# Optimization experiments

Measured on AMD Instinct MI355X. Metric: run time of the kernel, lower is better.

## Reference

```python
import jax, jax.numpy as jnp
import numpy as np

V = 50257   # vocab_size
H = 1024    # hidden_size + 8
L = 2048    # input_length
ML = 2048   # max_length


def setup_inputs() -> dict:
    key = jax.random.key(0)
    ks = jax.random.split(key, 12)
    def w(k, shape, scale=0.02):
        return jax.random.normal(k, shape, dtype=jnp.float32) * scale
    return {
        'decoder_input': jax.random.randint(ks[0], (1, 1), 0, V),
        'hidden_state': jax.random.normal(ks[1], (1, 1, H), dtype=jnp.float32),
        'encoder_outputs': jax.random.normal(ks[2], (ML, H), dtype=jnp.float32),
        'input_variable': jax.random.randint(ks[3], (L, 1), 0, V),
        'embedding': w(ks[4], (V, H), 1.0),
        'W_attn_w': w(ks[5], (ML, 2 * H)), 'b_attn_w': jnp.zeros((ML,), jnp.float32),
        'W_attn_u': w(ks[6], (H, 2 * H)), 'b_attn_u': jnp.zeros((H,), jnp.float32),
        'W_ih': w(ks[7], (3 * H, H)), 'b_ih': jnp.zeros((3 * H,), jnp.float32),
        'W_hh': w(ks[8], (3 * H, H)), 'b_hh': jnp.zeros((3 * H,), jnp.float32),
        'W_copy': w(ks[9], (H, H)), 'b_copy': jnp.zeros((H,), jnp.float32),
        'W_gen': w(ks[10], (V, H)), 'b_gen': jnp.zeros((V,), jnp.float32),
    }


def _forward(decoder_input, hidden_state, encoder_outputs, input_variable,
             embedding, W_attn_w, b_attn_w, W_attn_u, b_attn_u,
             W_ih, b_ih, W_hh, b_hh, W_copy, b_copy, W_gen, b_gen):
    # batch_size = 1, single decode step (dropout is identity at inference)
    emb0 = embedding[decoder_input].reshape(1, H)           # (1, H)
    h0 = hidden_state[0]                                    # (1, H) previous hidden

    # attention over encoder outputs
    cat_eh = jnp.concatenate([emb0, h0], axis=1)            # (1, 2H)
    attn_weights = jax.nn.softmax(cat_eh @ W_attn_w.T + b_attn_w, axis=1)  # (1, ML)
    attn_applied = attn_weights @ encoder_outputs           # (1, H)

    joined = jnp.concatenate([emb0, attn_applied], axis=1)  # (1, 2H)
    rnn_in = jax.nn.relu(joined @ W_attn_u.T + b_attn_u)    # (1, H)

    # one GRU step (PyTorch gate layout: r, z, n)
    gi = rnn_in @ W_ih.T + b_ih                             # (1, 3H)
    gh = h0 @ W_hh.T + b_hh                                 # (1, 3H)
    r = jax.nn.sigmoid(gi[:, :H] + gh[:, :H])
    z = jax.nn.sigmoid(gi[:, H:2 * H] + gh[:, H:2 * H])
    n = jnp.tanh(gi[:, 2 * H:] + r * gh[:, 2 * H:])
    h_new = (1.0 - z) * n + z * h0                          # (1, H)
    final_hidden = h_new[None]                              # (1, 1, H)

    # generate + copy scores
    score_g = h_new @ W_gen.T + b_gen                       # (1, V)
    trimmed = encoder_outputs[:L]                           # (L, H)
    score_c = jnp.tanh(trimmed @ W_copy.T + b_copy) @ h0[0] # (L,)  bmm with OLD hidden
    probs = jax.nn.softmax(jnp.concatenate([score_g, score_c[None]], axis=1), axis=1)
    prob_g = probs[:, :V]                                   # (1, V)
    prob_c = probs[:, V:]                                   # (1, L)

    # copy->vocab: scatter-add (math-equivalent to dense one-hot bmm)
    idx = input_variable[:, 0]                              # (L,) int
    prob_c_to_g = jnp.zeros((V,), probs.dtype).at[idx].add(prob_c[0])[None]
    final_output = prob_g + prob_c_to_g                     # (1, V)

    # selective read: attend only to positions matching the current input token
    din = decoder_input[0, 0]
    matched = (idx == din).astype(probs.dtype)              # (L,)
    final_weights = ((prob_c * matched) @ trimmed)[:, None, :]  # (1, 1, H)
    return final_output, final_hidden, final_weights


def reference(decoder_input, hidden_state, encoder_outputs, input_variable,
              embedding, W_attn_w, b_attn_w, W_attn_u, b_attn_u,
              W_ih, b_ih, W_hh, b_hh, W_copy, b_copy, W_gen, b_gen):
    return _forward(decoder_input, hidden_state, encoder_outputs, input_variable,
                    embedding, W_attn_w, b_attn_w, W_attn_u, b_attn_u,
                    W_ih, b_ih, W_hh, b_hh, W_copy, b_copy, W_gen, b_gen)
```

## Files before the change

### kernel.cpp

```cpp
#include <hip/hip_runtime.h>
#include <math.h>

#define VSZ 50257
#define HSZ 1024
#define LSZ 2048
#define SHIFT 60.0f

typedef __attribute__((ext_vector_type(8))) short bf16x8;
typedef __attribute__((ext_vector_type(4))) float f32x4;

__device__ __forceinline__ unsigned short f2bf(float f) {
  unsigned int u = __float_as_uint(f);
  u += 0x7FFFu + ((u >> 16) & 1u);
  return (unsigned short)(u >> 16);
}

__global__ void k_attn(const float* __restrict__ Waw, const float* __restrict__ baw,
                       const int* __restrict__ din, const float* __restrict__ emb,
                       const float* __restrict__ h0, const float* __restrict__ enc,
                       const float* __restrict__ Wc, float* __restrict__ attnw,
                       float* __restrict__ out, float* __restrict__ score_c,
                       float* __restrict__ acc, float* __restrict__ psum,
                       unsigned short* __restrict__ bfbuf) {
  int bid = blockIdx.x, tid = threadIdx.x;
  if (bid < 512) {
    int gw = bid * 4 + (tid >> 6);
    int lane = tid & 63;
    const float4* row = (const float4*)(Waw + (size_t)gw * 2048);
    const float4* e4 = (const float4*)(emb + (size_t)din[0] * HSZ);
    const float4* h4 = (const float4*)h0;
    float s = 0.f;
#pragma unroll
    for (int j = 0; j < 4; ++j) {
      float4 a = row[lane + 64 * j];
      float4 b = e4[lane + 64 * j];
      s += a.x * b.x + a.y * b.y + a.z * b.z + a.w * b.w;
    }
#pragma unroll
    for (int j = 0; j < 4; ++j) {
      float4 a = row[256 + lane + 64 * j];
      float4 b = h4[lane + 64 * j];
      s += a.x * b.x + a.y * b.y + a.z * b.z + a.w * b.w;
    }
#pragma unroll
    for (int o = 32; o > 0; o >>= 1) s += __shfl_down(s, o, 64);
    if (lane == 0) attnw[gw] = s + baw[gw];
  } else if (bid < 709) {
    int v = (bid - 512) * 256 + tid;
    if (v < VSZ) out[v] = 0.f;
  } else if (bid == 709) {
#pragma unroll
    for (int k = 0; k < 8; ++k) score_c[tid + 256 * k] = 0.f;
  } else if (bid == 710) {
#pragma unroll
    for (int k = 0; k < 4; ++k) acc[tid + 256 * k] = 0.f;
    if (tid == 0) psum[0] = 0.f;
  } else {
    int cb = bid - 711;
#pragma unroll
    for (int c = 0; c < 4; ++c) {
      int g = cb * 1024 + c * 256 + tid;
      float4 v;
      if (g < 524288) v = ((const float4*)enc)[g];
      else            v = ((const float4*)Wc)[g - 524288];
      ushort4 o;
      o.x = f2bf(v.x); o.y = f2bf(v.y); o.z = f2bf(v.z); o.w = f2bf(v.w);
      *(ushort4*)(bfbuf + (size_t)g * 4) = o;
    }
  }
}

__global__ void k_attn_apply(const float* __restrict__ attnw, const float* __restrict__ enc,
                             float* __restrict__ acc) {
  __shared__ float red[256];
  __shared__ float sw[64];
  int bid = blockIdx.x, t = threadIdx.x;
  int hb = bid & 3, mb = bid >> 2;
  float m = -1e30f;
  for (int i = t; i < LSZ; i += 256) m = fmaxf(m, attnw[i]);
  red[t] = m; __syncthreads();
  for (int s = 128; s > 0; s >>= 1) { if (t < s) red[t] = fmaxf(red[t], red[t + s]); __syncthreads(); }
  float gmax = red[0]; __syncthreads();
  float sum = 0.f;
  for (int i = t; i < LSZ; i += 256) sum += expf(attnw[i] - gmax);
  red[t] = sum; __syncthreads();
  for (int s = 128; s > 0; s >>= 1) { if (t < s) red[t] += red[t + s]; __syncthreads(); }
  float inv = 1.f / red[0];
  if (t < 64) sw[t] = expf(attnw[mb * 64 + t] - gmax) * inv;
  __syncthreads();
  int h = hb * 256 + t;
  float s = 0.f;
#pragma unroll 4
  for (int j = 0; j < 64; ++j) s = fmaf(sw[j], enc[(size_t)(mb * 64 + j) * HSZ + h], s);
  atomicAdd(&acc[h], s);
}

__global__ void k_rnn(const float* __restrict__ Wau, const float* __restrict__ bau,
                      const int* __restrict__ din, const float* __restrict__ emb,
                      const float* __restrict__ acc, float* __restrict__ rnn_in) {
  int gw = blockIdx.x * 4 + (threadIdx.x >> 6);
  int lane = threadIdx.x & 63;
  const float4* row = (const float4*)(Wau + (size_t)gw * 2048);
  const float4* e4 = (const float4*)(emb + (size_t)din[0] * HSZ);
  const float4* a4 = (const float4*)acc;
  float s = 0.f;
#pragma unroll
  for (int j = 0; j < 4; ++j) {
    float4 a = row[lane + 64 * j];
    float4 b = e4[lane + 64 * j];
    s += a.x * b.x + a.y * b.y + a.z * b.z + a.w * b.w;
  }
#pragma unroll
  for (int j = 0; j < 4; ++j) {
    float4 a = row[256 + lane + 64 * j];
    float4 b = a4[lane + 64 * j];
    s += a.x * b.x + a.y * b.y + a.z * b.z + a.w * b.w;
  }
#pragma unroll
  for (int o = 32; o > 0; o >>= 1) s += __shfl_down(s, o, 64);
  if (lane == 0) rnn_in[gw] = fmaxf(s + bau[gw], 0.f);
}

__global__ void k_gates(const float* __restrict__ Wih, const float* __restrict__ bih,
                        const float* __restrict__ xin, const float* __restrict__ Whh,
                        const float* __restrict__ bhh, const float* __restrict__ h0,
                        float* __restrict__ y) {
  int gw = blockIdx.x * 4 + (threadIdx.x >> 6);
  int lane = threadIdx.x & 63;
  const float* W; const float* x; float bv; int r;
  if (gw < 3 * HSZ) { W = Wih; x = xin; r = gw; bv = bih[r]; }
  else              { W = Whh; x = h0;  r = gw - 3 * HSZ; bv = bhh[r]; }
  const float4* row = (const float4*)(W + (size_t)r * HSZ);
  const float4* xv = (const float4*)x;
  float s = 0.f;
#pragma unroll
  for (int j = 0; j < 4; ++j) {
    float4 a = row[lane + 64 * j];
    float4 b = xv[lane + 64 * j];
    s += a.x * b.x + a.y * b.y + a.z * b.z + a.w * b.w;
  }
#pragma unroll
  for (int o = 32; o > 0; o >>= 1) s += __shfl_down(s, o, 64);
  if (lane == 0) y[gw] = s + bv;
}

__global__ void k_gru(const float* __restrict__ gi, const float* __restrict__ gh,
                      const float* __restrict__ h0, float* __restrict__ h_new,
                      float* __restrict__ out) {
  int t = blockIdx.x * 256 + threadIdx.x;
  float r = 1.f / (1.f + expf(-(gi[t] + gh[t])));
  float z = 1.f / (1.f + expf(-(gi[HSZ + t] + gh[HSZ + t])));
  float n = tanhf(gi[2 * HSZ + t] + r * gh[2 * HSZ + t]);
  float hn = (1.f - z) * n + z * h0[t];
  h_new[t] = hn;
  out[VSZ + t] = hn;
  out[VSZ + HSZ + t] = 0.f;
}

__global__ __launch_bounds__(256) void k_huge(
    const unsigned short* __restrict__ encB, const unsigned short* __restrict__ WcB,
    const float* __restrict__ bc, const float* __restrict__ hvec,
    const float* __restrict__ Wg, const float* __restrict__ bg,
    const float* __restrict__ h_new, float* __restrict__ score) {
  int bid = blockIdx.x, tid = threadIdx.x;
  int wave = tid >> 6, lane = tid & 63;
  if (bid < 512) {
    int l0 = (bid >> 4) * 64 + wave * 16;
    int h0r = (bid & 15) * 64;
    int col = lane & 15, quad = lane >> 4;
    f32x4 acc[4] = {};
    const unsigned short* arow = encB + ((size_t)(l0 + col) << 10) + quad * 8;
#pragma unroll 4
    for (int k0 = 0; k0 < HSZ; k0 += 32) {
      bf16x8 a = *(const bf16x8*)(arow + k0);
#pragma unroll
      for (int ht = 0; ht < 4; ++ht) {
        bf16x8 b = *(const bf16x8*)(WcB + ((size_t)(h0r + ht * 16 + col) << 10) + k0 + quad * 8);
        acc[ht] = __builtin_amdgcn_mfma_f32_16x16x32_bf16(a, b, acc[ht], 0, 0, 0);
      }
    }
    float rsum[4] = {0.f, 0.f, 0.f, 0.f};
#pragma unroll
    for (int ht = 0; ht < 4; ++ht) {
      int h = h0r + ht * 16 + col;
      float bch = bc[h], hw = hvec[h];
#pragma unroll
      for (int r = 0; r < 4; ++r) rsum[r] += tanhf(acc[ht][r] + bch) * hw;
    }
#pragma unroll
    for (int o = 1; o < 16; o <<= 1) {
#pragma unroll
      for (int r = 0; r < 4; ++r) rsum[r] += __shfl_xor(rsum[r], o, 64);
    }
    if (col == 0) {
      int lrow = l0 + quad * 4;
#pragma unroll
      for (int r = 0; r < 4; ++r) atomicAdd(&score[VSZ + lrow + r], rsum[r]);
    }
  } else {
    int r0 = (bid - 512) * 8 + wave * 2;
    int ra = r0 < VSZ ? r0 : VSZ - 1;
    int rb = r0 + 1 < VSZ ? r0 + 1 : VSZ - 1;
    const float4* xv = (const float4*)h_new;
    float4 x0 = xv[lane], x1 = xv[lane + 64], x2 = xv[lane + 128], x3 = xv[lane + 192];
    const float4* p0 = (const float4*)(Wg + (size_t)ra * HSZ);
    const float4* p1 = (const float4*)(Wg + (size_t)rb * HSZ);
    float4 a0 = p0[lane], a1 = p0[lane + 64], a2 = p0[lane + 128], a3 = p0[lane + 192];
    float4 b0 = p1[lane], b1 = p1[lane + 64], b2 = p1[lane + 128], b3 = p1[lane + 192];
    float s0 = a0.x * x0.x + a0.y * x0.y + a0.z * x0.z + a0.w * x0.w
             + a1.x * x1.x + a1.y * x1.y + a1.z * x1.z + a1.w * x1.w
             + a2.x * x2.x + a2.y * x2.y + a2.z * x2.z + a2.w * x2.w
             + a3.x * x3.x + a3.y * x3.y + a3.z * x3.z + a3.w * x3.w;
    float s1 = b0.x * x0.x + b0.y * x0.y + b0.z * x0.z + b0.w * x0.w
             + b1.x * x1.x + b1.y * x1.y + b1.z * x1.z + b1.w * x1.w
             + b2.x * x2.x + b2.y * x2.y + b2.z * x2.z + b2.w * x2.w
             + b3.x * x3.x + b3.y * x3.y + b3.z * x3.z + b3.w * x3.w;
#pragma unroll
    for (int o = 32; o > 0; o >>= 1) {
      s0 += __shfl_down(s0, o, 64);
      s1 += __shfl_down(s1, o, 64);
    }
    if (lane == 0) {
      if (r0 < VSZ) score[r0] = s0 + bg[r0];
      if (r0 + 1 < VSZ) score[r0 + 1] = s1 + bg[r0 + 1];
    }
  }
}

__global__ void k_sum(const float* __restrict__ score, float* __restrict__ psum) {
  __shared__ float sh[256];
  int t = threadIdx.x, b = blockIdx.x;
  float s = 0.f;
  for (int i = b * 256 + t; i < VSZ + LSZ; i += 64 * 256) s += expf(score[i] - SHIFT);
  sh[t] = s; __syncthreads();
  for (int s2 = 128; s2 > 0; s2 >>= 1) { if (t < s2) sh[t] += sh[t + s2]; __syncthreads(); }
  if (t == 0) atomicAdd(psum, sh[0]);
}

__global__ void k_final(const float* __restrict__ score, const float* __restrict__ psum,
                        const int* __restrict__ idx, const int* __restrict__ din,
                        const float* __restrict__ enc, float* __restrict__ out) {
  int bid = blockIdx.x, t = threadIdx.x;
  float inv = 1.f / psum[0];
  if (bid < 197) {
    int v = bid * 256 + t;
    if (v < VSZ) atomicAdd(&out[v], expf(score[v] - SHIFT) * inv);
  } else {
    __shared__ float pm[256];
    __shared__ int flag;
    if (t == 0) flag = 0;
    __syncthreads();
    int l0 = (bid - 197) * 256;
    int l = l0 + t;
    float p = expf(score[VSZ + l] - SHIFT) * inv;
    atomicAdd(&out[idx[l]], p);
    int matched = (idx[l] == din[0]);
    pm[t] = matched ? p : 0.f;
    if (matched) atomicExch(&flag, 1);
    __syncthreads();
    if (flag) {
      for (int h = t; h < HSZ; h += 256) {
        float s = 0.f;
        for (int l2 = 0; l2 < 256; ++l2)
          if (pm[l2] != 0.f) s = fmaf(pm[l2], enc[(size_t)(l0 + l2) * HSZ + h], s);
        if (s != 0.f) atomicAdd(&out[VSZ + HSZ + h], s);
      }
    }
  }
}

extern "C" void kernel_launch(void* const* d_in, const int* in_sizes, int n_in,
                              void* d_out, int out_size, void* d_ws, size_t ws_size,
                              hipStream_t stream) {
  const int*   din = (const int*)d_in[0];
  const float* h0  = (const float*)d_in[1];
  const float* enc = (const float*)d_in[2];
  const int*   idx = (const int*)d_in[3];
  const float* emb = (const float*)d_in[4];
  const float* Waw = (const float*)d_in[5];
  const float* baw = (const float*)d_in[6];
  const float* Wau = (const float*)d_in[7];
  const float* bau = (const float*)d_in[8];
  const float* Wih = (const float*)d_in[9];
  const float* bih = (const float*)d_in[10];
  const float* Whh = (const float*)d_in[11];
  const float* bhh = (const float*)d_in[12];
  const float* Wc  = (const float*)d_in[13];
  const float* bc  = (const float*)d_in[14];
  const float* Wg  = (const float*)d_in[15];
  const float* bg  = (const float*)d_in[16];
  float* out = (float*)d_out;
  float* ws  = (float*)d_ws;

  float* acc    = ws;
  float* rnn_in = ws + 1024;
  float* gi     = ws + 2048;
  float* h_new  = ws + 8192;
  float* attnw  = ws + 9216;
  float* score  = ws + 11264;
  float* psum   = ws + 63616;
  unsigned short* bfbuf = (unsigned short*)(ws + 64000);
  unsigned short* encB = bfbuf;
  unsigned short* WcB  = bfbuf + 2097152;

  k_attn<<<1479, 256, 0, stream>>>(Waw, baw, din, emb, h0, enc, Wc, attnw, out,
                                   score + VSZ, acc, psum, bfbuf);
  k_attn_apply<<<128, 256, 0, stream>>>(attnw, enc, acc);
  k_rnn<<<256, 256, 0, stream>>>(Wau, bau, din, emb, acc, rnn_in);
  k_gates<<<1536, 256, 0, stream>>>(Wih, bih, rnn_in, Whh, bhh, h0, gi);
  k_gru<<<4, 256, 0, stream>>>(gi, gi + 3072, h0, h_new, out);
  k_huge<<<512 + (VSZ + 7) / 8, 256, 0, stream>>>(encB, WcB, bc, h0, Wg, bg, h_new, score);
  k_sum<<<64, 256, 0, stream>>>(score, psum);
  k_final<<<205, 256, 0, stream>>>(score, psum, idx, din, enc, out);
}
```

Before: 463.5 us.

## Hoist independent GEMVs into prologue, fuse GRU and softmax sum into main kernel

The W_hh·h0 gate GEMV and the embedding half of the attn_u GEMV now run in the first kernel, since neither depends on the attention result, so the critical path after attention gets shorter. The GRU elementwise step is recomputed per block inside the big vocab kernel, and the exp-sum is accumulated there into 64 spread atomic slots, which removes the k_gru and k_sum launches. The copy-score GEMM is retiled so each block covers 16 rows over all of H, which lets it write scores directly instead of using atomics. In exchange, every GEMV block redundantly recomputes the 1024-element GRU update, and the GEMM now uses fewer blocks, each doing more serial work.

```diff
diff --git a/kernel.cpp b/kernel.cpp
--- a/kernel.cpp
+++ b/kernel.cpp
@@ -5,6 +5,8 @@
 #define HSZ 1024
 #define LSZ 2048
 #define SHIFT 60.0f
+#define NGEMM 128
+#define NGEMV 6283
 
 typedef __attribute__((ext_vector_type(8))) short bf16x8;
 typedef __attribute__((ext_vector_type(4))) float f32x4;
@@ -15,48 +17,55 @@
   return (unsigned short)(u >> 16);
 }
 
-__global__ void k_attn(const float* __restrict__ Waw, const float* __restrict__ baw,
-                       const int* __restrict__ din, const float* __restrict__ emb,
-                       const float* __restrict__ h0, const float* __restrict__ enc,
-                       const float* __restrict__ Wc, float* __restrict__ attnw,
-                       float* __restrict__ out, float* __restrict__ score_c,
-                       float* __restrict__ acc, float* __restrict__ psum,
-                       unsigned short* __restrict__ bfbuf) {
+__device__ __forceinline__ float dot256(const float4* __restrict__ row,
+                                        const float4* __restrict__ x, int lane) {
+  float s = 0.f;
+#pragma unroll
+  for (int j = 0; j < 4; ++j) {
+    float4 a = row[lane + 64 * j];
+    float4 b = x[lane + 64 * j];
+    s += a.x * b.x + a.y * b.y + a.z * b.z + a.w * b.w;
+  }
+  return s;
+}
+
+__global__ void k_pre(const float* __restrict__ Waw, const float* __restrict__ baw,
+                      const int* __restrict__ din, const float* __restrict__ emb,
+                      const float* __restrict__ h0, const float* __restrict__ enc,
+                      const float* __restrict__ Wc, const float* __restrict__ Whh,
+                      const float* __restrict__ bhh, const float* __restrict__ Wau,
+                      const float* __restrict__ bau, float* __restrict__ attnw,
+                      float* __restrict__ gh, float* __restrict__ part,
+                      float* __restrict__ out, float* __restrict__ psum,
+                      unsigned short* __restrict__ bfbuf) {
   int bid = blockIdx.x, tid = threadIdx.x;
+  int wave = tid >> 6, lane = tid & 63;
   if (bid < 512) {
-    int gw = bid * 4 + (tid >> 6);
-    int lane = tid & 63;
+    int gw = bid * 4 + wave;
     const float4* row = (const float4*)(Waw + (size_t)gw * 2048);
-    const float4* e4 = (const float4*)(emb + (size_t)din[0] * HSZ);
-    const float4* h4 = (const float4*)h0;
-    float s = 0.f;
-#pragma unroll
-    for (int j = 0; j < 4; ++j) {
-      float4 a = row[lane + 64 * j];
-      float4 b = e4[lane + 64 * j];
-      s += a.x * b.x + a.y * b.y + a.z * b.z + a.w * b.w;
-    }
-#pragma unroll
-    for (int j = 0; j < 4; ++j) {
-      float4 a = row[256 + lane + 64 * j];
-      float4 b = h4[lane + 64 * j];
-      s += a.x * b.x + a.y * b.y + a.z * b.z + a.w * b.w;
-    }
+    float s = dot256(row, (const float4*)(emb + (size_t)din[0] * HSZ), lane)
+            + dot256(row + 256, (const float4*)h0, lane);
 #pragma unroll
     for (int o = 32; o > 0; o >>= 1) s += __shfl_down(s, o, 64);
     if (lane == 0) attnw[gw] = s + baw[gw];
-  } else if (bid < 709) {
-    int v = (bid - 512) * 256 + tid;
+  } else if (bid < 1280) {
+    int gw = (bid - 512) * 4 + wave;
+    float s = dot256((const float4*)(Whh + (size_t)gw * HSZ), (const float4*)h0, lane);
+#pragma unroll
+    for (int o = 32; o > 0; o >>= 1) s += __shfl_down(s, o, 64);
+    if (lane == 0) gh[gw] = s + bhh[gw];
+  } else if (bid < 1536) {
+    int gw = (bid - 1280) * 4 + wave;
+    float s = dot256((const float4*)(Wau + (size_t)gw * 2048),
+                     (const float4*)(emb + (size_t)din[0] * HSZ), lane);
+#pragma unroll
+    for (int o = 32; o > 0; o >>= 1) s += __shfl_down(s, o, 64);
+    if (lane == 0) part[gw] = s + bau[gw];
+  } else if (bid < 1733) {
+    int v = (bid - 1536) * 256 + tid;
     if (v < VSZ) out[v] = 0.f;
-  } else if (bid == 709) {
-#pragma unroll
-    for (int k = 0; k < 8; ++k) score_c[tid + 256 * k] = 0.f;
-  } else if (bid == 710) {
-#pragma unroll
-    for (int k = 0; k < 4; ++k) acc[tid + 256 * k] = 0.f;
-    if (tid == 0) psum[0] = 0.f;
-  } else {
-    int cb = bid - 711;
+  } else if (bid < 2501) {
+    int cb = bid - 1733;
 #pragma unroll
     for (int c = 0; c < 4; ++c) {
       int g = cb * 1024 + c * 256 + tid;
@@ -67,6 +76,9 @@
       o.x = f2bf(v.x); o.y = f2bf(v.y); o.z = f2bf(v.z); o.w = f2bf(v.w);
       *(ushort4*)(bfbuf + (size_t)g * 4) = o;
     }
+  } else {
+#pragma unroll
+    for (int k = 0; k < 8; ++k) psum[tid + 256 * k] = 0.f;
   }
 }
 
@@ -92,116 +104,99 @@
   float s = 0.f;
 #pragma unroll 4
   for (int j = 0; j < 64; ++j) s = fmaf(sw[j], enc[(size_t)(mb * 64 + j) * HSZ + h], s);
-  atomicAdd(&acc[h], s);
-}
-
-__global__ void k_rnn(const float* __restrict__ Wau, const float* __restrict__ bau,
-                      const int* __restrict__ din, const float* __restrict__ emb,
-                      const float* __restrict__ acc, float* __restrict__ rnn_in) {
+  if (mb == 0) acc[h] = s;
+  else atomicAdd(&acc[h], s);
+}
+
+__global__ void k_rnn2(const float* __restrict__ Wau, const float* __restrict__ part,
+                       const float* __restrict__ acc, float* __restrict__ rnn_in) {
   int gw = blockIdx.x * 4 + (threadIdx.x >> 6);
   int lane = threadIdx.x & 63;
-  const float4* row = (const float4*)(Wau + (size_t)gw * 2048);
-  const float4* e4 = (const float4*)(emb + (size_t)din[0] * HSZ);
-  const float4* a4 = (const float4*)acc;
-  float s = 0.f;
-#pragma unroll
-  for (int j = 0; j < 4; ++j) {
-    float4 a = row[lane + 64 * j];
-    float4 b = e4[lane + 64 * j];
-    s += a.x * b.x + a.y * b.y + a.z * b.z + a.w * b.w;
-  }
-#pragma unroll
-  for (int j = 0; j < 4; ++j) {
-    float4 a = row[256 + lane + 64 * j];
-    float4 b = a4[lane + 64 * j];
-    s += a.x * b.x + a.y * b.y + a.z * b.z + a.w * b.w;
-  }
+  float s = dot256((const float4*)(Wau + (size_t)gw * 2048) + 256, (const float4*)acc, lane);
 #pragma unroll
   for (int o = 32; o > 0; o >>= 1) s += __shfl_down(s, o, 64);
-  if (lane == 0) rnn_in[gw] = fmaxf(s + bau[gw], 0.f);
-}
-
-__global__ void k_gates(const float* __restrict__ Wih, const float* __restrict__ bih,
-                        const float* __restrict__ xin, const float* __restrict__ Whh,
-                        const float* __restrict__ bhh, const float* __restrict__ h0,
-                        float* __restrict__ y) {
+  if (lane == 0) rnn_in[gw] = fmaxf(s + part[gw], 0.f);
+}
+
+__global__ void k_gi(const float* __restrict__ Wih, const float* __restrict__ bih,
+                     const float* __restrict__ rnn_in, float* __restrict__ gi) {
   int gw = blockIdx.x * 4 + (threadIdx.x >> 6);
   int lane = threadIdx.x & 63;
-  const float* W; const float* x; float bv; int r;
-  if (gw < 3 * HSZ) { W = Wih; x = xin; r = gw; bv = bih[r]; }
-  else              { W = Whh; x = h0;  r = gw - 3 * HSZ; bv = bhh[r]; }
-  const float4* row = (const float4*)(W + (size_t)r * HSZ);
-  const float4* xv = (const float4*)x;
-  float s = 0.f;
-#pragma unroll
-  for (int j = 0; j < 4; ++j) {
-    float4 a = row[lane + 64 * j];
-    float4 b = xv[lane + 64 * j];
-    s += a.x * b.x + a.y * b.y + a.z * b.z + a.w * b.w;
-  }
+  float s = dot256((const float4*)(Wih + (size_t)gw * HSZ), (const float4*)rnn_in, lane);
 #pragma unroll
   for (int o = 32; o > 0; o >>= 1) s += __shfl_down(s, o, 64);
-  if (lane == 0) y[gw] = s + bv;
-}
-
-__global__ void k_gru(const float* __restrict__ gi, const float* __restrict__ gh,
-                      const float* __restrict__ h0, float* __restrict__ h_new,
-                      float* __restrict__ out) {
-  int t = blockIdx.x * 256 + threadIdx.x;
-  float r = 1.f / (1.f + expf(-(gi[t] + gh[t])));
-  float z = 1.f / (1.f + expf(-(gi[HSZ + t] + gh[HSZ + t])));
-  float n = tanhf(gi[2 * HSZ + t] + r * gh[2 * HSZ + t]);
-  float hn = (1.f - z) * n + z * h0[t];
-  h_new[t] = hn;
-  out[VSZ + t] = hn;
-  out[VSZ + HSZ + t] = 0.f;
+  if (lane == 0) gi[gw] = s + bih[gw];
 }
 
 __global__ __launch_bounds__(256) void k_huge(
     const unsigned short* __restrict__ encB, const unsigned short* __restrict__ WcB,
     const float* __restrict__ bc, const float* __restrict__ hvec,
     const float* __restrict__ Wg, const float* __restrict__ bg,
-    const float* __restrict__ h_new, float* __restrict__ score) {
+    const float* __restrict__ gi, const float* __restrict__ gh,
+    const float* __restrict__ h0, float* __restrict__ score,
+    float* __restrict__ psum, float* __restrict__ out) {
   int bid = blockIdx.x, tid = threadIdx.x;
   int wave = tid >> 6, lane = tid & 63;
-  if (bid < 512) {
-    int l0 = (bid >> 4) * 64 + wave * 16;
-    int h0r = (bid & 15) * 64;
+  if (bid < NGEMM) {
+    __shared__ float sred[4][16];
+    int l0 = bid * 16;
     int col = lane & 15, quad = lane >> 4;
-    f32x4 acc[4] = {};
-    const unsigned short* arow = encB + ((size_t)(l0 + col) << 10) + quad * 8;
-#pragma unroll 4
-    for (int k0 = 0; k0 < HSZ; k0 += 32) {
-      bf16x8 a = *(const bf16x8*)(arow + k0);
-#pragma unroll
-      for (int ht = 0; ht < 4; ++ht) {
-        bf16x8 b = *(const bf16x8*)(WcB + ((size_t)(h0r + ht * 16 + col) << 10) + k0 + quad * 8);
+    int h0r = wave * 256;
+    f32x4 acc[16] = {};
+    const unsigned short* aw = encB + ((size_t)(l0 + col) << 10) + quad * 8;
+#pragma unroll
+    for (int ht = 0; ht < 16; ++ht) {
+      const unsigned short* bw = WcB + ((size_t)(h0r + ht * 16 + col) << 10) + quad * 8;
+#pragma unroll 8
+      for (int kk = 0; kk < 32; ++kk) {
+        bf16x8 a = *(const bf16x8*)(aw + kk * 32);
+        bf16x8 b = *(const bf16x8*)(bw + kk * 32);
         acc[ht] = __builtin_amdgcn_mfma_f32_16x16x32_bf16(a, b, acc[ht], 0, 0, 0);
       }
     }
     float rsum[4] = {0.f, 0.f, 0.f, 0.f};
 #pragma unroll
-    for (int ht = 0; ht < 4; ++ht) {
+    for (int ht = 0; ht < 16; ++ht) {
       int h = h0r + ht * 16 + col;
       float bch = bc[h], hw = hvec[h];
 #pragma unroll
       for (int r = 0; r < 4; ++r) rsum[r] += tanhf(acc[ht][r] + bch) * hw;
     }
 #pragma unroll
-    for (int o = 1; o < 16; o <<= 1) {
+    for (int o = 1; o < 16; o <<= 1)
 #pragma unroll
       for (int r = 0; r < 4; ++r) rsum[r] += __shfl_xor(rsum[r], o, 64);
-    }
     if (col == 0) {
-      int lrow = l0 + quad * 4;
-#pragma unroll
-      for (int r = 0; r < 4; ++r) atomicAdd(&score[VSZ + lrow + r], rsum[r]);
+#pragma unroll
+      for (int r = 0; r < 4; ++r) sred[wave][quad * 4 + r] = rsum[r];
+    }
+    __syncthreads();
+    if (tid < 16) {
+      float s = sred[0][tid] + sred[1][tid] + sred[2][tid] + sred[3][tid];
+      score[VSZ + l0 + tid] = s;
+      float e = expf(s - SHIFT);
+#pragma unroll
+      for (int o = 1; o < 16; o <<= 1) e += __shfl_xor(e, o, 64);
+      if (tid == 0) atomicAdd(&psum[((bid * 37) & 63) * 32], e);
     }
   } else {
-    int r0 = (bid - 512) * 8 + wave * 2;
+    __shared__ float xs[HSZ];
+    __shared__ float es[4];
+#pragma unroll
+    for (int j = 0; j < 4; ++j) {
+      int i = tid + 256 * j;
+      float r = 1.f / (1.f + expf(-(gi[i] + gh[i])));
+      float z = 1.f / (1.f + expf(-(gi[HSZ + i] + gh[HSZ + i])));
+      float n = tanhf(gi[2 * HSZ + i] + r * gh[2 * HSZ + i]);
+      float hn = (1.f - z) * n + z * h0[i];
+      xs[i] = hn;
+      if (bid == NGEMM) { out[VSZ + i] = hn; out[VSZ + HSZ + i] = 0.f; }
+    }
+    __syncthreads();
+    int r0 = (bid - NGEMM) * 8 + wave * 2;
     int ra = r0 < VSZ ? r0 : VSZ - 1;
     int rb = r0 + 1 < VSZ ? r0 + 1 : VSZ - 1;
-    const float4* xv = (const float4*)h_new;
+    const float4* xv = (const float4*)xs;
     float4 x0 = xv[lane], x1 = xv[lane + 64], x2 = xv[lane + 128], x3 = xv[lane + 192];
     const float4* p0 = (const float4*)(Wg + (size_t)ra * HSZ);
     const float4* p1 = (const float4*)(Wg + (size_t)rb * HSZ);
@@ -221,27 +216,30 @@
       s1 += __shfl_down(s1, o, 64);
     }
     if (lane == 0) {
-      if (r0 < VSZ) score[r0] = s0 + bg[r0];
-      if (r0 + 1 < VSZ) score[r0 + 1] = s1 + bg[r0 + 1];
-    }
-  }
-}
-
-__global__ void k_sum(const float* __restrict__ score, float* __restrict__ psum) {
-  __shared__ float sh[256];
-  int t = threadIdx.x, b = blockIdx.x;
-  float s = 0.f;
-  for (int i = b * 256 + t; i < VSZ + LSZ; i += 64 * 256) s += expf(score[i] - SHIFT);
-  sh[t] = s; __syncthreads();
-  for (int s2 = 128; s2 > 0; s2 >>= 1) { if (t < s2) sh[t] += sh[t + s2]; __syncthreads(); }
-  if (t == 0) atomicAdd(psum, sh[0]);
+      float e = 0.f;
+      if (r0 < VSZ)     { float v = s0 + bg[r0];     score[r0] = v;     e += expf(v - SHIFT); }
+      if (r0 + 1 < VSZ) { float v = s1 + bg[r0 + 1]; score[r0 + 1] = v; e += expf(v - SHIFT); }
+      es[wave] = e;
+    }
+    __syncthreads();
+    if (tid == 0)
+      atomicAdd(&psum[((bid * 37) & 63) * 32], es[0] + es[1] + es[2] + es[3]);
+  }
 }
 
 __global__ void k_final(const float* __restrict__ score, const float* __restrict__ psum,
                         const int* __restrict__ idx, const int* __restrict__ din,
                         const float* __restrict__ enc, float* __restrict__ out) {
+  __shared__ float sinv;
   int bid = blockIdx.x, t = threadIdx.x;
-  float inv = 1.f / psum[0];
+  if (t < 64) {
+    float v = psum[t * 32];
+#pragma unroll
+    for (int o = 1; o < 64; o <<= 1) v += __shfl_xor(v, o, 64);
+    if (t == 0) sinv = 1.f / v;
+  }
+  __syncthreads();
+  float inv = sinv;
   if (bid < 197) {
     int v = bid * 256 + t;
     if (v < VSZ) atomicAdd(&out[v], expf(score[v] - SHIFT) * inv);
@@ -293,23 +291,23 @@
   float* ws  = (float*)d_ws;
 
   float* acc    = ws;
-  float* rnn_in = ws + 1024;
-  float* gi     = ws + 2048;
-  float* h_new  = ws + 8192;
+  float* part   = ws + 1024;
+  float* rnn_in = ws + 2048;
+  float* gi     = ws + 3072;
+  float* gh     = ws + 6144;
   float* attnw  = ws + 9216;
   float* score  = ws + 11264;
   float* psum   = ws + 63616;
-  unsigned short* bfbuf = (unsigned short*)(ws + 64000);
+  unsigned short* bfbuf = (unsigned short*)(ws + 65664);
   unsigned short* encB = bfbuf;
   unsigned short* WcB  = bfbuf + 2097152;
 
-  k_attn<<<1479, 256, 0, stream>>>(Waw, baw, din, emb, h0, enc, Wc, attnw, out,
-                                   score + VSZ, acc, psum, bfbuf);
+  k_pre<<<2502, 256, 0, stream>>>(Waw, baw, din, emb, h0, enc, Wc, Whh, bhh, Wau, bau,
+                                  attnw, gh, part, out, psum, bfbuf);
   k_attn_apply<<<128, 256, 0, stream>>>(attnw, enc, acc);
-  k_rnn<<<256, 256, 0, stream>>>(Wau, bau, din, emb, acc, rnn_in);
-  k_gates<<<1536, 256, 0, stream>>>(Wih, bih, rnn_in, Whh, bhh, h0, gi);
-  k_gru<<<4, 256, 0, stream>>>(gi, gi + 3072, h0, h_new, out);
-  k_huge<<<512 + (VSZ + 7) / 8, 256, 0, stream>>>(encB, WcB, bc, h0, Wg, bg, h_new, score);
-  k_sum<<<64, 256, 0, stream>>>(score, psum);
+  k_rnn2<<<256, 256, 0, stream>>>(Wau, part, acc, rnn_in);
+  k_gi<<<768, 256, 0, stream>>>(Wih, bih, rnn_in, gi);
+  k_huge<<<NGEMM + NGEMV, 256, 0, stream>>>(encB, WcB, bc, h0, Wg, bg, gi, gh, h0,
+                                            score, psum, out);
   k_final<<<205, 256, 0, stream>>>(score, psum, idx, din, enc, out);
 }
```

After: 524.5 us. +13.2%, slower.
